# Optimization experiments

Measured on AMD Instinct MI355X. Metric: run time of the kernel, lower is better.

## Reference

```python
import jax, jax.numpy as jnp
import numpy as np

GRID_SIZE = 8
POSITIVE_MARGIN = 1.0
NEGATIVE_MARGIN = 0.2
LAMBDA_D = 250.0
B, Hc, Wc, D = 4, 60, 60, 64


def warp_points(points, homographies):
    """points: [N,2] in (y,x); homographies: [B,3,3]. Returns [B,N,2] in (y,x)."""
    n = points.shape[0]
    xy1 = jnp.concatenate([points[:, ::-1], jnp.ones((n, 1), points.dtype)], axis=-1)  # (x,y,1)
    w = jnp.einsum('bij,nj->bni', homographies, xy1)  # [B,N,3]
    w = w[..., :2] / w[..., 2:3]
    return w[..., ::-1]  # back to (y,x)


def setup_inputs() -> dict:
    key = jax.random.key(0)
    k1, k2, k3 = jax.random.split(key, 3)
    descriptors = jax.random.normal(k1, (B, Hc, Wc, D), dtype=jnp.float32)
    warped_descriptors = jax.random.normal(k2, (B, Hc, Wc, D), dtype=jnp.float32)
    # near-identity homographies so warped cell centers remain close to the grid
    homographies = jnp.eye(3, dtype=jnp.float32)[None] + 0.001 * jax.random.normal(
        k3, (B, 3, 3), dtype=jnp.float32)
    valid_mask = jnp.ones((B, Hc * GRID_SIZE, Wc * GRID_SIZE), dtype=jnp.float32)
    return {"descriptors": descriptors, "warped_descriptors": warped_descriptors,
            "homographies": homographies, "valid_mask": valid_mask}


def reference(descriptors, warped_descriptors, homographies, valid_mask):
    b, hc, wc, d = descriptors.shape
    g = GRID_SIZE

    # cell-center coordinates (y, x) at full resolution
    yy, xx = jnp.meshgrid(jnp.arange(hc), jnp.arange(wc), indexing='ij')
    coord_cells = jnp.stack([yy, xx], axis=-1).astype(jnp.float32) * g + g // 2  # [Hc,Wc,2]

    warped_coord_cells = warp_points(coord_cells.reshape(-1, 2), homographies)  # [B,Hc*Wc,2]
    cc = coord_cells.reshape(1, 1, 1, hc, wc, 2)
    wcc = warped_coord_cells.reshape(b, hc, wc, 1, 1, 2)
    cell_distances = jnp.linalg.norm(cc - wcc, axis=-1)  # [B,Hc,Wc,Hc,Wc]
    s = (cell_distances <= g - 0.5).astype(descriptors.dtype)

    # broadcast dot-product score tensor [B,Hc,Wc,Hc,Wc]
    dot = jnp.einsum('bijd,bkld->bijkl', descriptors, warped_descriptors)

    positive_dist = jnp.maximum(0.0, POSITIVE_MARGIN - dot)
    negative_dist = jnp.maximum(0.0, dot - NEGATIVE_MARGIN)
    loss = LAMBDA_D * s * positive_dist + (1.0 - s) * negative_dist

    # space-to-depth + prod over the g*g block == per-cell AND of the valid mask
    vm = valid_mask.reshape(b, hc, g, wc, g)
    vm = jnp.prod(vm, axis=(2, 4))  # [B,Hc,Wc]
    vm = vm.reshape(b, 1, 1, hc, wc)

    normalization = jnp.sum(vm) * jnp.float32(hc * wc)
    return jnp.sum(vm * loss) / normalization
```

## Files before the change

### kernel.cpp

```cpp
#include <hip/hip_runtime.h>
#include <hip/hip_bf16.h>

#define HC 60
#define WCC 60
#define DD 64
#define NCELL (HC * WCC)
#define NBC (4 * NCELL)
#define IMG (HC * 8)
#define MPAD 3840
#define NT2 30

#define CVT_BLOCKS 480
#define VM_BLOCKS 57
#define WC_BLOCKS 60
#define PREP_BLOCKS (CVT_BLOCKS + VM_BLOCKS + WC_BLOCKS)
#define GEMM_BLOCKS (NT2 * NT2 * 4)

typedef __bf16 bf16x8 __attribute__((ext_vector_type(8)));
typedef float f32x4 __attribute__((ext_vector_type(4)));
typedef unsigned short u16x8 __attribute__((ext_vector_type(8)));

__device__ inline unsigned short f2bf(float f) {
    union { float f; unsigned u; } x; x.f = f;
    unsigned u = x.u;
    unsigned r = (u + 0x7fffu + ((u >> 16) & 1u)) >> 16;
    return (unsigned short)r;
}

__device__ inline void gload_lds16(const void* g, void* l) {
    __builtin_amdgcn_global_load_lds(
        (const __attribute__((address_space(1))) unsigned int*)g,
        (__attribute__((address_space(3))) unsigned int*)l, 16, 0, 0);
}

__device__ inline int div60(int v) { return (v * 17477) >> 20; }

__global__ __launch_bounds__(256) void dl_prep_kernel(
    const float* __restrict__ desc, const float* __restrict__ wdesc,
    const float* __restrict__ homog, const float* __restrict__ mask,
    unsigned short* __restrict__ descb, unsigned short* __restrict__ wdescb,
    float* __restrict__ vm, float* __restrict__ vpart, float2* __restrict__ wcent)
{
    const int bid = blockIdx.x;
    const int tid = threadIdx.x;

    if (bid < CVT_BLOCKS) {
        int t = bid * 256 + tid;
        int brow = t >> 3;
        int col = (t & 7) * 8;
        int b = brow / MPAD;
        int row = brow - b * MPAD;
        u16x8 oa = (u16x8)0, ob = (u16x8)0;
        if (row < NCELL) {
            size_t src = ((size_t)(b * NCELL + row)) * DD + col;
            float4 a0 = *(const float4*)(desc + src);
            float4 a1 = *(const float4*)(desc + src + 4);
            float4 b0 = *(const float4*)(wdesc + src);
            float4 b1 = *(const float4*)(wdesc + src + 4);
            oa[0] = f2bf(a0.x); oa[1] = f2bf(a0.y); oa[2] = f2bf(a0.z); oa[3] = f2bf(a0.w);
            oa[4] = f2bf(a1.x); oa[5] = f2bf(a1.y); oa[6] = f2bf(a1.z); oa[7] = f2bf(a1.w);
            ob[0] = f2bf(b0.x); ob[1] = f2bf(b0.y); ob[2] = f2bf(b0.z); ob[3] = f2bf(b0.w);
            ob[4] = f2bf(b1.x); ob[5] = f2bf(b1.y); ob[6] = f2bf(b1.z); ob[7] = f2bf(b1.w);
        }
        size_t dst = (size_t)brow * DD + col;
        *(u16x8*)(descb + dst) = oa;
        *(u16x8*)(wdescb + dst) = ob;
    } else if (bid < CVT_BLOCKS + VM_BLOCKS) {
        int vb = bid - CVT_BLOCKS;
        int cell = vb * 256 + tid;
        float v = 0.f;
        if (cell < NBC) {
            int b = cell / NCELL;
            int rem = cell % NCELL;
            int k = rem / WCC, l = rem % WCC;
            const float* p = mask + (size_t)b * IMG * IMG + (size_t)(k * 8) * IMG + l * 8;
            float prod = 1.f;
#pragma unroll
            for (int dy = 0; dy < 8; ++dy) {
                float4 a0 = *(const float4*)(p + (size_t)dy * IMG);
                float4 a1 = *(const float4*)(p + (size_t)dy * IMG + 4);
                prod *= a0.x * a0.y * a0.z * a0.w * a1.x * a1.y * a1.z * a1.w;
            }
            vm[cell] = prod;
            v = prod;
        }
#pragma unroll
        for (int off = 32; off > 0; off >>= 1) v += __shfl_xor(v, off);
        __shared__ float sp[4];
        if ((tid & 63) == 0) sp[tid >> 6] = v;
        __syncthreads();
        if (tid == 0) vpart[vb] = sp[0] + sp[1] + sp[2] + sp[3];
    } else {
        int t = (bid - CVT_BLOCKS - VM_BLOCKS) * 256 + tid;
        int b = t / MPAD;
        int r = t - b * MPAD;
        float2 o;
        if (r < NCELL) {
            int i = div60(r);
            int j = r - i * WCC;
            const float* H = homog + b * 9;
            float x = (float)(j * 8 + 4), y = (float)(i * 8 + 4);
            float X2 = H[6] * x + H[7] * y + H[8];
            o.x = (H[3] * x + H[4] * y + H[5]) / X2;
            o.y = (H[0] * x + H[1] * y + H[2]) / X2;
        } else {
            o.x = 1e9f; o.y = 1e9f;
        }
        wcent[t] = o;
    }
}

__global__ __launch_bounds__(256, 3) void dl_gemm_loss_kernel(
    const unsigned short* __restrict__ descb, const unsigned short* __restrict__ wdescb,
    const float* __restrict__ vm, const float2* __restrict__ wcent,
    float* __restrict__ gpart)
{
    __shared__ unsigned char sA[128 * 128];
    __shared__ unsigned char sB[128 * 128];
    __shared__ float2 swc[128];
    __shared__ float swave[4];

    const int b = blockIdx.z;
    const int m0 = blockIdx.x * 128;
    const int n0 = blockIdx.y * 128;
    const int tid = threadIdx.x;
    const int lane = tid & 63;
    const int wv = tid >> 6;

    const unsigned char* gA = (const unsigned char*)(descb + (size_t)b * MPAD * DD) + (size_t)m0 * 128;
    const unsigned char* gB = (const unsigned char*)(wdescb + (size_t)b * MPAD * DD) + (size_t)n0 * 128;

    {
        const int swz = ((lane & 7) ^ (lane >> 3)) << 4;
        const int lrow = lane >> 3;
#pragma unroll
        for (int t = 0; t < 4; ++t) {
            int row = wv * 32 + t * 8 + lrow;
            gload_lds16(gA + (size_t)row * 128 + swz, sA + wv * 4096 + t * 1024);
            gload_lds16(gB + (size_t)row * 128 + swz, sB + wv * 4096 + t * 1024);
        }
    }
    if (tid < 128) swc[tid] = wcent[b * MPAD + m0 + tid];

    const int wr = wv >> 1, wc = wv & 1;
    const int frow = lane & 15;
    const int kg = (lane >> 4) * 16;

    float cyv[4], cxv[4], vmv[4];
#pragma unroll
    for (int fj = 0; fj < 4; ++fj) {
        int col = n0 + wc * 64 + fj * 16 + frow;
        int k = div60(col);
        int l = col - k * WCC;
        cyv[fj] = (float)(k * 8 + 4);
        cxv[fj] = (float)(l * 8 + 4);
        vmv[fj] = (col < NCELL) ? vm[b * NCELL + col] : 0.f;
    }
    float wyl = wcent[b * MPAD + m0 + wr * 64 + lane].x;
    float wlo = wyl, whi = wyl;
#pragma unroll
    for (int off = 32; off > 0; off >>= 1) {
        wlo = fminf(wlo, __shfl_xor(wlo, off));
        whi = fmaxf(whi, __shfl_xor(whi, off));
    }
    int c0 = n0 + wc * 64;
    float cy0 = (float)(div60(c0) * 8 + 4) - 7.5f;
    float cy1 = (float)(div60(c0 + 63) * 8 + 4) + 7.5f;
    bool full = (whi >= cy0) && (wlo <= cy1);

    __syncthreads();

    f32x4 acc[4][4];
#pragma unroll
    for (int i2 = 0; i2 < 4; ++i2)
#pragma unroll
        for (int j2 = 0; j2 < 4; ++j2)
            acc[i2][j2] = (f32x4)(0.f);

#pragma unroll
    for (int kk = 0; kk < 2; ++kk) {
        int kbyte = kk * 64 + kg;
        bf16x8 afr[4], bfr[4];
#pragma unroll
        for (int f = 0; f < 4; ++f) {
            int ra = wr * 64 + f * 16 + frow;
            afr[f] = *(const bf16x8*)(sA + ra * 128 + (kbyte ^ ((ra & 7) << 4)));
            int rb = wc * 64 + f * 16 + frow;
            bfr[f] = *(const bf16x8*)(sB + rb * 128 + (kbyte ^ ((rb & 7) << 4)));
        }
#pragma unroll
        for (int fi = 0; fi < 4; ++fi)
#pragma unroll
            for (int fj = 0; fj < 4; ++fj)
                acc[fi][fj] = __builtin_amdgcn_mfma_f32_16x16x32_bf16(
                    afr[fi], bfr[fj], acc[fi][fj], 0, 0, 0);
    }

    float partial = 0.f;
    if (full) {
#pragma unroll
        for (int fi = 0; fi < 4; ++fi) {
#pragma unroll
            for (int q = 0; q < 4; ++q) {
                float2 w2 = swc[wr * 64 + fi * 16 + (lane >> 4) * 4 + q];
#pragma unroll
                for (int fj = 0; fj < 4; ++fj) {
                    float dot = acc[fi][fj][q];
                    float ddy = cyv[fj] - w2.x;
                    float ddx = cxv[fj] - w2.y;
                    float d2 = ddy * ddy + ddx * ddx;
                    float pos = 250.f * fmaxf(1.f - dot, 0.f) + 0.2f;
                    float neg = fmaxf(dot, 0.2f);
                    partial += vmv[fj] * ((d2 <= 56.25f) ? pos : neg);
                }
            }
        }
    } else {
#pragma unroll
        for (int fj = 0; fj < 4; ++fj) {
            float cs = 0.f;
#pragma unroll
            for (int fi = 0; fi < 4; ++fi)
#pragma unroll
                for (int q = 0; q < 4; ++q)
                    cs += fmaxf(acc[fi][fj][q], 0.2f);
            partial = fmaf(vmv[fj], cs, partial);
        }
    }

#pragma unroll
    for (int off = 32; off > 0; off >>= 1) partial += __shfl_xor(partial, off);
    if (lane == 0) swave[wv] = partial;
    __syncthreads();
    if (tid == 0)
        gpart[blockIdx.x + NT2 * (blockIdx.y + NT2 * b)] =
            swave[0] + swave[1] + swave[2] + swave[3];
}

__global__ __launch_bounds__(256) void dl_final_kernel(
    const float* __restrict__ vpart, const float* __restrict__ gpart,
    float* __restrict__ out)
{
    int tid = threadIdx.x;
    float ls = 0.f, vs = 0.f;
    for (int i = tid; i < GEMM_BLOCKS; i += 256) ls += gpart[i];
    for (int i = tid; i < VM_BLOCKS; i += 256) vs += vpart[i];
#pragma unroll
    for (int off = 32; off > 0; off >>= 1) {
        ls += __shfl_xor(ls, off);
        vs += __shfl_xor(vs, off);
    }
    __shared__ float sl[4], sv[4];
    if ((tid & 63) == 0) { sl[tid >> 6] = ls; sv[tid >> 6] = vs; }
    __syncthreads();
    if (tid == 0) {
        float L = sl[0] + sl[1] + sl[2] + sl[3];
        float V = sv[0] + sv[1] + sv[2] + sv[3];
        L -= 0.2f * (float)MPAD * V;
        out[0] = L / (V * (float)NCELL);
    }
}

extern "C" void kernel_launch(void* const* d_in, const int* in_sizes, int n_in,
                              void* d_out, int out_size, void* d_ws, size_t ws_size,
                              hipStream_t stream) {
    const float* desc  = (const float*)d_in[0];
    const float* wdesc = (const float*)d_in[1];
    const float* homog = (const float*)d_in[2];
    const float* mask  = (const float*)d_in[3];
    float* out = (float*)d_out;
    float* wsf = (float*)d_ws;

    float* vpart = wsf;
    float* vm    = wsf + 64;
    float* gpart = wsf + 64 + NBC;
    float2* wcent = (float2*)(wsf + 18064);
    unsigned short* descb  = (unsigned short*)(wsf + 49408);
    unsigned short* wdescb = descb + (size_t)4 * MPAD * DD;

    hipLaunchKernelGGL(dl_prep_kernel, dim3(PREP_BLOCKS), dim3(256), 0, stream,
                       desc, wdesc, homog, mask, descb, wdescb, vm, vpart, wcent);
    hipLaunchKernelGGL(dl_gemm_loss_kernel, dim3(NT2, NT2, 4), dim3(256), 0, stream,
                       descb, wdescb, vm, wcent, gpart);
    hipLaunchKernelGGL(dl_final_kernel, dim3(1), dim3(256), 0, stream,
                       vpart, gpart, out);
}
```

Before: 36.71 us.

## Persistent GEMM blocks with A-tile reuse, B double-buffering, and fused final reduction

Replaces the one-block-per-tile grid of 3600 blocks with 768 persistent blocks that each walk a contiguous range of tiles. A blocks are reused across consecutive tiles that share the same row. The next B tile is prefetched into a second LDS buffer while the current tile is computed. The separate final-reduction kernel is removed; the last block to finish, found through an atomic counter reset in the prep kernel, does the final sum. This cuts block launch overhead, redundant A loads and one kernel launch, at the cost of extra LDS, serialised per-block work and the reliance on an atomic/threadfence pattern.

```diff
diff --git a/kernel.cpp b/kernel.cpp
--- a/kernel.cpp
+++ b/kernel.cpp
@@ -9,12 +9,13 @@
 #define IMG (HC * 8)
 #define MPAD 3840
 #define NT2 30
+#define NTILES (NT2 * NT2 * 4)
+#define GB 768
 
 #define CVT_BLOCKS 480
 #define VM_BLOCKS 57
 #define WC_BLOCKS 60
 #define PREP_BLOCKS (CVT_BLOCKS + VM_BLOCKS + WC_BLOCKS)
-#define GEMM_BLOCKS (NT2 * NT2 * 4)
 
 typedef __bf16 bf16x8 __attribute__((ext_vector_type(8)));
 typedef float f32x4 __attribute__((ext_vector_type(4)));
@@ -39,7 +40,8 @@
     const float* __restrict__ desc, const float* __restrict__ wdesc,
     const float* __restrict__ homog, const float* __restrict__ mask,
     unsigned short* __restrict__ descb, unsigned short* __restrict__ wdescb,
-    float* __restrict__ vm, float* __restrict__ vpart, float2* __restrict__ wcent)
+    float* __restrict__ vm, float* __restrict__ vpart, float2* __restrict__ wcent,
+    unsigned int* __restrict__ done)
 {
     const int bid = blockIdx.x;
     const int tid = threadIdx.x;
@@ -91,6 +93,7 @@
         __syncthreads();
         if (tid == 0) vpart[vb] = sp[0] + sp[1] + sp[2] + sp[3];
     } else {
+        if (bid == CVT_BLOCKS + VM_BLOCKS && tid == 0) *done = 0u;
         int t = (bid - CVT_BLOCKS - VM_BLOCKS) * 256 + tid;
         int b = t / MPAD;
         int r = t - b * MPAD;
@@ -113,151 +116,194 @@
 __global__ __launch_bounds__(256, 3) void dl_gemm_loss_kernel(
     const unsigned short* __restrict__ descb, const unsigned short* __restrict__ wdescb,
     const float* __restrict__ vm, const float2* __restrict__ wcent,
-    float* __restrict__ gpart)
+    const float* __restrict__ vpart,
+    float* __restrict__ gpart, unsigned int* __restrict__ done,
+    float* __restrict__ out)
 {
-    __shared__ unsigned char sA[128 * 128];
-    __shared__ unsigned char sB[128 * 128];
+    __shared__ unsigned char sA[16384];
+    __shared__ unsigned char sB[2][16384];
     __shared__ float2 swc[128];
-    __shared__ float swave[4];
-
-    const int b = blockIdx.z;
-    const int m0 = blockIdx.x * 128;
-    const int n0 = blockIdx.y * 128;
+    __shared__ float sred[8];
+    __shared__ unsigned int slast;
+
     const int tid = threadIdx.x;
     const int lane = tid & 63;
     const int wv = tid >> 6;
-
-    const unsigned char* gA = (const unsigned char*)(descb + (size_t)b * MPAD * DD) + (size_t)m0 * 128;
-    const unsigned char* gB = (const unsigned char*)(wdescb + (size_t)b * MPAD * DD) + (size_t)n0 * 128;
-
-    {
-        const int swz = ((lane & 7) ^ (lane >> 3)) << 4;
-        const int lrow = lane >> 3;
-#pragma unroll
-        for (int t = 0; t < 4; ++t) {
-            int row = wv * 32 + t * 8 + lrow;
-            gload_lds16(gA + (size_t)row * 128 + swz, sA + wv * 4096 + t * 1024);
-            gload_lds16(gB + (size_t)row * 128 + swz, sB + wv * 4096 + t * 1024);
-        }
-    }
-    if (tid < 128) swc[tid] = wcent[b * MPAD + m0 + tid];
-
-    const int wr = wv >> 1, wc = wv & 1;
+    const int p = blockIdx.x;
+    const int t0 = (NTILES * p) / GB;
+    const int t1 = (NTILES * (p + 1)) / GB;
+
+    const int wr = wv >> 1, wcs = wv & 1;
     const int frow = lane & 15;
     const int kg = (lane >> 4) * 16;
-
-    float cyv[4], cxv[4], vmv[4];
-#pragma unroll
-    for (int fj = 0; fj < 4; ++fj) {
-        int col = n0 + wc * 64 + fj * 16 + frow;
-        int k = div60(col);
-        int l = col - k * WCC;
-        cyv[fj] = (float)(k * 8 + 4);
-        cxv[fj] = (float)(l * 8 + 4);
-        vmv[fj] = (col < NCELL) ? vm[b * NCELL + col] : 0.f;
+    const int swz = ((lane & 7) ^ (lane >> 3)) << 4;
+    const int lrow = lane >> 3;
+
+    float partial = 0.f;
+    float wlo = 0.f, whi = 0.f;
+    int pb = 0;
+    int curax = -1;
+
+    for (int t = t0; t < t1; ++t) {
+        int b = t / (NT2 * NT2);
+        int r = t - b * (NT2 * NT2);
+        int x = r / NT2;
+        int y = r - x * NT2;
+        int axkey = b * 32 + x;
+
+        if (axkey != curax) {
+            const unsigned char* gA = (const unsigned char*)(descb + (size_t)b * MPAD * DD)
+                                      + (size_t)(x * 128) * 128;
+            const unsigned char* gB = (const unsigned char*)(wdescb + (size_t)b * MPAD * DD)
+                                      + (size_t)(y * 128) * 128;
+#pragma unroll
+            for (int q = 0; q < 4; ++q) {
+                int row = wv * 32 + q * 8 + lrow;
+                gload_lds16(gA + (size_t)row * 128 + swz, sA + wv * 4096 + q * 1024);
+                gload_lds16(gB + (size_t)row * 128 + swz, sB[pb] + wv * 4096 + q * 1024);
+            }
+            if (tid < 128) swc[tid] = wcent[b * MPAD + x * 128 + tid];
+            float wyl = wcent[b * MPAD + x * 128 + wr * 64 + lane].x;
+            wlo = wyl; whi = wyl;
+#pragma unroll
+            for (int off = 32; off > 0; off >>= 1) {
+                wlo = fminf(wlo, __shfl_xor(wlo, off));
+                whi = fmaxf(whi, __shfl_xor(whi, off));
+            }
+            curax = axkey;
+            __syncthreads();
+        }
+
+        bool pref = false;
+        {
+            int tn = t + 1;
+            if (tn < t1) {
+                int bn = tn / (NT2 * NT2);
+                int rn = tn - bn * (NT2 * NT2);
+                int xn = rn / NT2;
+                int yn = rn - xn * NT2;
+                if (bn * 32 + xn == curax) {
+                    const unsigned char* gBn =
+                        (const unsigned char*)(wdescb + (size_t)bn * MPAD * DD)
+                        + (size_t)(yn * 128) * 128;
+#pragma unroll
+                    for (int q = 0; q < 4; ++q) {
+                        int row = wv * 32 + q * 8 + lrow;
+                        gload_lds16(gBn + (size_t)row * 128 + swz,
+                                    sB[pb ^ 1] + wv * 4096 + q * 1024);
+                    }
+                    pref = true;
+                }
+            }
+        }
+
+        int n0 = y * 128;
+        float cyv[4], cxv[4], vmv[4];
+#pragma unroll
+        for (int fj = 0; fj < 4; ++fj) {
+            int col = n0 + wcs * 64 + fj * 16 + frow;
+            int k = div60(col);
+            int l = col - k * WCC;
+            cyv[fj] = (float)(k * 8 + 4);
+            cxv[fj] = (float)(l * 8 + 4);
+            vmv[fj] = (col < NCELL) ? vm[b * NCELL + col] : 0.f;
+        }
+        int c0 = n0 + wcs * 64;
+        float cy0 = (float)(div60(c0) * 8 + 4) - 7.5f;
+        float cy1 = (float)(div60(c0 + 63) * 8 + 4) + 7.5f;
+        bool full = (whi >= cy0) && (wlo <= cy1);
+
+        f32x4 acc[4][4];
+#pragma unroll
+        for (int i2 = 0; i2 < 4; ++i2)
+#pragma unroll
+            for (int j2 = 0; j2 < 4; ++j2)
+                acc[i2][j2] = (f32x4)(0.f);
+
+        const unsigned char* bB = sB[pb];
+#pragma unroll
+        for (int kk = 0; kk < 2; ++kk) {
+            int kbyte = kk * 64 + kg;
+            bf16x8 afr[4], bfr[4];
+#pragma unroll
+            for (int f = 0; f < 4; ++f) {
+                int ra = wr * 64 + f * 16 + frow;
+                afr[f] = *(const bf16x8*)(sA + ra * 128 + (kbyte ^ ((ra & 7) << 4)));
+                int rb = wcs * 64 + f * 16 + frow;
+                bfr[f] = *(const bf16x8*)(bB + rb * 128 + (kbyte ^ ((rb & 7) << 4)));
+            }
+#pragma unroll
+            for (int fi = 0; fi < 4; ++fi)
+#pragma unroll
+                for (int fj = 0; fj < 4; ++fj)
+                    acc[fi][fj] = __builtin_amdgcn_mfma_f32_16x16x32_bf16(
+                        afr[fi], bfr[fj], acc[fi][fj], 0, 0, 0);
+        }
+
+        if (full) {
+#pragma unroll
+            for (int fi = 0; fi < 4; ++fi) {
+#pragma unroll
+                for (int q = 0; q < 4; ++q) {
+                    float2 w2 = swc[wr * 64 + fi * 16 + (lane >> 4) * 4 + q];
+#pragma unroll
+                    for (int fj = 0; fj < 4; ++fj) {
+                        float dot = acc[fi][fj][q];
+                        float ddy = cyv[fj] - w2.x;
+                        float ddx = cxv[fj] - w2.y;
+                        float d2 = ddy * ddy + ddx * ddx;
+                        float pos = 250.f * fmaxf(1.f - dot, 0.f) + 0.2f;
+                        float neg = fmaxf(dot, 0.2f);
+                        partial += vmv[fj] * ((d2 <= 56.25f) ? pos : neg);
+                    }
+                }
+            }
+        } else {
+#pragma unroll
+            for (int fj = 0; fj < 4; ++fj) {
+                float cs = 0.f;
+#pragma unroll
+                for (int fi = 0; fi < 4; ++fi)
+#pragma unroll
+                    for (int q = 0; q < 4; ++q)
+                        cs += fmaxf(acc[fi][fj][q], 0.2f);
+                partial = fmaf(vmv[fj], cs, partial);
+            }
+        }
+
+        __syncthreads();
+        if (pref) pb ^= 1;
     }
-    float wyl = wcent[b * MPAD + m0 + wr * 64 + lane].x;
-    float wlo = wyl, whi = wyl;
-#pragma unroll
-    for (int off = 32; off > 0; off >>= 1) {
-        wlo = fminf(wlo, __shfl_xor(wlo, off));
-        whi = fmaxf(whi, __shfl_xor(whi, off));
-    }
-    int c0 = n0 + wc * 64;
-    float cy0 = (float)(div60(c0) * 8 + 4) - 7.5f;
-    float cy1 = (float)(div60(c0 + 63) * 8 + 4) + 7.5f;
-    bool full = (whi >= cy0) && (wlo <= cy1);
-
-    __syncthreads();
-
-    f32x4 acc[4][4];
-#pragma unroll
-    for (int i2 = 0; i2 < 4; ++i2)
-#pragma unroll
-        for (int j2 = 0; j2 < 4; ++j2)
-            acc[i2][j2] = (f32x4)(0.f);
-
-#pragma unroll
-    for (int kk = 0; kk < 2; ++kk) {
-        int kbyte = kk * 64 + kg;
-        bf16x8 afr[4], bfr[4];
-#pragma unroll
-        for (int f = 0; f < 4; ++f) {
-            int ra = wr * 64 + f * 16 + frow;
-            afr[f] = *(const bf16x8*)(sA + ra * 128 + (kbyte ^ ((ra & 7) << 4)));
-            int rb = wc * 64 + f * 16 + frow;
-            bfr[f] = *(const bf16x8*)(sB + rb * 128 + (kbyte ^ ((rb & 7) << 4)));
-        }
-#pragma unroll
-        for (int fi = 0; fi < 4; ++fi)
-#pragma unroll
-            for (int fj = 0; fj < 4; ++fj)
-                acc[fi][fj] = __builtin_amdgcn_mfma_f32_16x16x32_bf16(
-                    afr[fi], bfr[fj], acc[fi][fj], 0, 0, 0);
-    }
-
-    float partial = 0.f;
-    if (full) {
-#pragma unroll
-        for (int fi = 0; fi < 4; ++fi) {
-#pragma unroll
-            for (int q = 0; q < 4; ++q) {
-                float2 w2 = swc[wr * 64 + fi * 16 + (lane >> 4) * 4 + q];
-#pragma unroll
-                for (int fj = 0; fj < 4; ++fj) {
-                    float dot = acc[fi][fj][q];
-                    float ddy = cyv[fj] - w2.x;
-                    float ddx = cxv[fj] - w2.y;
-                    float d2 = ddy * ddy + ddx * ddx;
-                    float pos = 250.f * fmaxf(1.f - dot, 0.f) + 0.2f;
-                    float neg = fmaxf(dot, 0.2f);
-                    partial += vmv[fj] * ((d2 <= 56.25f) ? pos : neg);
-                }
-            }
-        }
-    } else {
-#pragma unroll
-        for (int fj = 0; fj < 4; ++fj) {
-            float cs = 0.f;
-#pragma unroll
-            for (int fi = 0; fi < 4; ++fi)
-#pragma unroll
-                for (int q = 0; q < 4; ++q)
-                    cs += fmaxf(acc[fi][fj][q], 0.2f);
-            partial = fmaf(vmv[fj], cs, partial);
-        }
-    }
 
 #pragma unroll
     for (int off = 32; off > 0; off >>= 1) partial += __shfl_xor(partial, off);
-    if (lane == 0) swave[wv] = partial;
-    __syncthreads();
-    if (tid == 0)
-        gpart[blockIdx.x + NT2 * (blockIdx.y + NT2 * b)] =
-            swave[0] + swave[1] + swave[2] + swave[3];
-}
-
-__global__ __launch_bounds__(256) void dl_final_kernel(
-    const float* __restrict__ vpart, const float* __restrict__ gpart,
-    float* __restrict__ out)
-{
-    int tid = threadIdx.x;
-    float ls = 0.f, vs = 0.f;
-    for (int i = tid; i < GEMM_BLOCKS; i += 256) ls += gpart[i];
-    for (int i = tid; i < VM_BLOCKS; i += 256) vs += vpart[i];
-#pragma unroll
-    for (int off = 32; off > 0; off >>= 1) {
-        ls += __shfl_xor(ls, off);
-        vs += __shfl_xor(vs, off);
-    }
-    __shared__ float sl[4], sv[4];
-    if ((tid & 63) == 0) { sl[tid >> 6] = ls; sv[tid >> 6] = vs; }
+    if (lane == 0) sred[wv] = partial;
     __syncthreads();
     if (tid == 0) {
-        float L = sl[0] + sl[1] + sl[2] + sl[3];
-        float V = sv[0] + sv[1] + sv[2] + sv[3];
-        L -= 0.2f * (float)MPAD * V;
-        out[0] = L / (V * (float)NCELL);
+        gpart[p] = sred[0] + sred[1] + sred[2] + sred[3];
+        __threadfence();
+        slast = atomicAdd(done, 1u);
+    }
+    __syncthreads();
+    if (slast == GB - 1) {
+        __threadfence();
+        float ls = 0.f, vs = 0.f;
+        for (int i = tid; i < GB; i += 256) ls += gpart[i];
+        for (int i = tid; i < VM_BLOCKS; i += 256) vs += vpart[i];
+#pragma unroll
+        for (int off = 32; off > 0; off >>= 1) {
+            ls += __shfl_xor(ls, off);
+            vs += __shfl_xor(vs, off);
+        }
+        __shared__ float sl[4], sv[4];
+        if ((tid & 63) == 0) { sl[tid >> 6] = ls; sv[tid >> 6] = vs; }
+        __syncthreads();
+        if (tid == 0) {
+            float L = sl[0] + sl[1] + sl[2] + sl[3];
+            float V = sv[0] + sv[1] + sv[2] + sv[3];
+            L -= 0.2f * (float)MPAD * V;
+            out[0] = L / (V * (float)NCELL);
+        }
     }
 }
 
@@ -274,14 +320,13 @@
     float* vpart = wsf;
     float* vm    = wsf + 64;
     float* gpart = wsf + 64 + NBC;
-    float2* wcent = (float2*)(wsf + 18064);
-    unsigned short* descb  = (unsigned short*)(wsf + 49408);
+    unsigned int* done = (unsigned int*)(wsf + 15296);
+    float2* wcent = (float2*)(wsf + 15304);
+    unsigned short* descb  = (unsigned short*)(wsf + 46080);
     unsigned short* wdescb = descb + (size_t)4 * MPAD * DD;
 
     hipLaunchKernelGGL(dl_prep_kernel, dim3(PREP_BLOCKS), dim3(256), 0, stream,
-                       desc, wdesc, homog, mask, descb, wdescb, vm, vpart, wcent);
-    hipLaunchKernelGGL(dl_gemm_loss_kernel, dim3(NT2, NT2, 4), dim3(256), 0, stream,
-                       descb, wdescb, vm, wcent, gpart);
-    hipLaunchKernelGGL(dl_final_kernel, dim3(1), dim3(256), 0, stream,
-                       vpart, gpart, out);
-}
+                       desc, wdesc, homog, mask, descb, wdescb, vm, vpart, wcent, done);
+    hipLaunchKernelGGL(dl_gemm_loss_kernel, dim3(GB), dim3(256), 0, stream,
+                       descb, wdescb, vm, wcent, vpart, gpart, done, out);
+}
```

Measured after the change: 44.02 us. 1.2x slower.
